# Kernel optimization log

Measured on AMD Instinct MI355X. Metric: run time of the kernel, lower is better.

Reference implementation:

```python
import jax, jax.numpy as jnp
import numpy as np

B, NQ, NK, QS, KS, H, VD = 16, 64, 512, 256, 256, 256, 256


def setup_inputs() -> dict:
    key = jax.random.key(0)
    k1, k2, k3, k4, k5, k6, k7 = jax.random.split(key, 7)
    return {
        "queries": jax.random.normal(k1, (B, NQ, QS), dtype=jnp.float32),
        "keys": jax.random.normal(k2, (B, NK, KS), dtype=jnp.float32),
        "values": jax.random.normal(k3, (B, NK, VD), dtype=jnp.float32),
        "valid_lens": jax.random.randint(k4, (B,), 1, NK + 1, dtype=jnp.int32),
        # learned params (nn.Linear with bias=False): W_q [QS,H], W_k [KS,H], w_v [H]
        "W_q": jax.random.normal(k5, (QS, H), dtype=jnp.float32) / np.sqrt(QS),
        "W_k": jax.random.normal(k6, (KS, H), dtype=jnp.float32) / np.sqrt(KS),
        "w_v": jax.random.normal(k7, (H,), dtype=jnp.float32) / np.sqrt(H),
    }


def reference(queries, keys, values, valid_lens, W_q, W_k, w_v):
    # project: q [B,nq,H], k [B,nk,H]
    q = jnp.einsum("bqd,dh->bqh", queries, W_q)
    k = jnp.einsum("bkd,dh->bkh", keys, W_k)
    # broadcast-add -> tanh -> score reduction via w_v: [B,nq,nk]
    features = jnp.tanh(q[:, :, None, :] + k[:, None, :, :])  # [B,nq,nk,H]
    scores = jnp.einsum("bqkh,h->bqk", features, w_v)
    # masked softmax over keys (positions >= valid_len masked out)
    mask = jnp.arange(scores.shape[-1])[None, None, :] < valid_lens[:, None, None]
    scores = jnp.where(mask, scores, -1e6)
    attn = jax.nn.softmax(scores, axis=-1)
    # weighted sum of values (dropout p=0 / eval mode => identity)
    return jnp.einsum("bqk,bkv->bqv", attn, values)
```

## Files before the change

kernel.cpp:

```cpp
#include <hip/hip_runtime.h>
#include <hip/hip_bf16.h>

#define BB 16
#define NQ 64
#define NK 512
#define HD 256

typedef __attribute__((ext_vector_type(8))) short short8;
typedef __attribute__((ext_vector_type(4))) float f32x4;

__device__ __forceinline__ ushort bf16_rne(float v) {
    unsigned u = __float_as_uint(v);
    return (ushort)((u + 0x7FFFu + ((u >> 16) & 1u)) >> 16);
}
__device__ __forceinline__ float bf16_to_f(ushort h) {
    return __uint_as_float(((unsigned)h) << 16);
}

__global__ __launch_bounds__(256) void wconv(
    const float* __restrict__ wq, const float* __restrict__ wk,
    ushort* __restrict__ wqh, ushort* __restrict__ wql,
    ushort* __restrict__ wkh, ushort* __restrict__ wkl)
{
    int widx = blockIdx.x * 256 + threadIdx.x;
    const float* W; ushort *wh, *wl;
    if (widx < 16384) { W = wq; wh = wqh; wl = wql; }
    else { W = wk; wh = wkh; wl = wkl; widx -= 16384; }
    int n  = widx >> 6;
    int k4 = (widx & 63) * 4;
    ushort hh[4], ll[4];
    #pragma unroll
    for (int c = 0; c < 4; ++c) {
        float v = W[(k4 + c) * 256 + n];
        hh[c] = bf16_rne(v);
        ll[c] = bf16_rne(v - bf16_to_f(hh[c]));
    }
    *(ushort4*)&wh[n * 256 + k4] = make_ushort4(hh[0], hh[1], hh[2], hh[3]);
    *(ushort4*)&wl[n * 256 + k4] = make_ushort4(ll[0], ll[1], ll[2], ll[3]);
}

__global__ __launch_bounds__(256, 2) void proj_fused(
    const float* __restrict__ queries, const float* __restrict__ keys,
    const ushort* __restrict__ wqh, const ushort* __restrict__ wql,
    const ushort* __restrict__ wkh, const ushort* __restrict__ wkl,
    float* __restrict__ qp, float* __restrict__ kp, float scale)
{
    __shared__ ushort AsH[64 * 64], AsL[64 * 64];
    __shared__ ushort BsH[64 * 64], BsL[64 * 64];

    const float* A; const ushort *Bh, *Bl; float* C; int rows0;
    const int bx = blockIdx.x;
    if (bx < 16) { A = queries; Bh = wqh; Bl = wql; C = qp; rows0 = bx * 64; }
    else         { A = keys;    Bh = wkh; Bl = wkl; C = kp; rows0 = (bx - 16) * 64; }
    const int cols0 = blockIdx.y * 64;

    const int t = threadIdx.x, lane = t & 63, wave = t >> 6;
    const int quad = lane >> 4, l15 = lane & 15;
    const int sr  = t >> 2;
    const int sc2 = (t & 3) * 2;

    f32x4 acc[4];
    #pragma unroll
    for (int j = 0; j < 4; ++j) acc[j] = (f32x4){0.f, 0.f, 0.f, 0.f};

    for (int k0 = 0; k0 < 256; k0 += 64) {
        const float* arow = &A[(size_t)(rows0 + sr) * 256 + k0 + sc2 * 8];
        float4 a0 = *(const float4*)&arow[0];
        float4 a1 = *(const float4*)&arow[4];
        float4 a2 = *(const float4*)&arow[8];
        float4 a3 = *(const float4*)&arow[12];
        const ushort* bhp = &Bh[(size_t)(cols0 + sr) * 256 + k0 + sc2 * 8];
        const ushort* blp = &Bl[(size_t)(cols0 + sr) * 256 + k0 + sc2 * 8];
        short8 b0h = *(const short8*)&bhp[0];
        short8 b1h = *(const short8*)&bhp[8];
        short8 b0l = *(const short8*)&blp[0];
        short8 b1l = *(const short8*)&blp[8];

        __syncthreads();

        float av[16] = {a0.x, a0.y, a0.z, a0.w, a1.x, a1.y, a1.z, a1.w,
                        a2.x, a2.y, a2.z, a2.w, a3.x, a3.y, a3.z, a3.w};
        short8 ah0, ah1, al0, al1;
        #pragma unroll
        for (int e = 0; e < 8; ++e) {
            ushort h0 = bf16_rne(av[e]);
            ushort h1 = bf16_rne(av[8 + e]);
            ah0[e] = (short)h0;
            ah1[e] = (short)h1;
            al0[e] = (short)bf16_rne(av[e] - bf16_to_f(h0));
            al1[e] = (short)bf16_rne(av[8 + e] - bf16_to_f(h1));
        }
        {
            int s0 = sr * 8 + ((sc2 + 0) ^ (sr & 7));
            int s1 = sr * 8 + ((sc2 + 1) ^ (sr & 7));
            *(short8*)&AsH[s0 * 8] = ah0;
            *(short8*)&AsH[s1 * 8] = ah1;
            *(short8*)&AsL[s0 * 8] = al0;
            *(short8*)&AsL[s1 * 8] = al1;
            *(short8*)&BsH[s0 * 8] = b0h;
            *(short8*)&BsH[s1 * 8] = b1h;
            *(short8*)&BsL[s0 * 8] = b0l;
            *(short8*)&BsL[s1 * 8] = b1l;
        }
        __syncthreads();

        #pragma unroll
        for (int ks = 0; ks < 2; ++ks) {
            const int c = ks * 4 + quad;
            short8 aH, aL, bH[4], bL[4];
            {
                int r = wave * 16 + l15;
                int slot = r * 8 + (c ^ (r & 7));
                aH = *(const short8*)&AsH[slot * 8];
                aL = *(const short8*)&AsL[slot * 8];
            }
            #pragma unroll
            for (int ns = 0; ns < 4; ++ns) {
                int n = ns * 16 + l15;
                int slot = n * 8 + (c ^ (n & 7));
                bH[ns] = *(const short8*)&BsH[slot * 8];
                bL[ns] = *(const short8*)&BsL[slot * 8];
            }
            #pragma unroll
            for (int ns = 0; ns < 4; ++ns)
                acc[ns] = __builtin_amdgcn_mfma_f32_16x16x32_bf16(aH, bH[ns], acc[ns], 0, 0, 0);
            #pragma unroll
            for (int ns = 0; ns < 4; ++ns)
                acc[ns] = __builtin_amdgcn_mfma_f32_16x16x32_bf16(aL, bH[ns], acc[ns], 0, 0, 0);
            #pragma unroll
            for (int ns = 0; ns < 4; ++ns)
                acc[ns] = __builtin_amdgcn_mfma_f32_16x16x32_bf16(aH, bL[ns], acc[ns], 0, 0, 0);
        }
    }

    const int rbase = rows0 + wave * 16 + quad * 4;
    #pragma unroll
    for (int ns = 0; ns < 4; ++ns) {
        int col = cols0 + ns * 16 + l15;
        #pragma unroll
        for (int r = 0; r < 4; ++r)
            C[(size_t)(rbase + r) * 256 + col] =
                __builtin_amdgcn_exp2f(acc[ns][r] * scale);
    }
}

__global__ __launch_bounds__(256, 3) void score_pv_seg4(
    const float* __restrict__ qp,
    const float* __restrict__ kp,
    const float* __restrict__ values,
    const int*   __restrict__ vlens,
    const float* __restrict__ w_v,
    float* __restrict__ pO,
    float* __restrict__ pL)
{
    __shared__ float eq[8][260];
    __shared__ float wv[HD];
    __shared__ float Ps[8][66];
    __shared__ float part[4][8][260];

    const int b   = blockIdx.x & 15;
    const int qt  = blockIdx.x >> 4;
    const int seg = blockIdx.y;
    const int vl  = vlens[b];
    if (seg * 64 >= vl) return;

    const int t = threadIdx.x, lane = t & 63, wave = t >> 6;
    const int key = wave * 16 + (lane >> 2);
    const int ch  = lane & 3;
    const int kg  = seg * 64 + key;

    const float* krow = kp + ((size_t)b * NK + kg) * HD + ch * 4;
    float4 ek[16];
    #pragma unroll
    for (int j = 0; j < 16; ++j) ek[j] = *(const float4*)&krow[j * 16];

    const float* qsrc = qp + ((size_t)b * NQ + qt * 8) * HD;
    #pragma unroll
    for (int i = 0; i < 2; ++i) {
        int idx = i * 256 + t;
        int row = idx >> 6, c4 = (idx & 63) * 4;
        *(float4*)&eq[row][c4] = *(const float4*)&qsrc[(size_t)row * HD + c4];
    }
    if (t < 64) *(float4*)&wv[t * 4] = *(const float4*)&w_v[t * 4];
    __syncthreads();

    float Wsum;
    {
        float ws = wv[lane] + wv[lane + 64] + wv[lane + 128] + wv[lane + 192];
        #pragma unroll
        for (int off = 32; off; off >>= 1) ws += __shfl_xor(ws, off);
        Wsum = ws;
    }

    float s[8] = {0.f, 0.f, 0.f, 0.f, 0.f, 0.f, 0.f, 0.f};
    #pragma unroll
    for (int j = 0; j < 16; ++j) {
        const int h = j * 16 + ch * 4;
        float4 e4 = ek[j];
        float4 w4 = *(const float4*)&wv[h];
        #pragma unroll
        for (int qi = 0; qi < 8; ++qi) {
            float4 q4 = *(const float4*)&eq[qi][h];
            float p0 = fmaf(q4.x, e4.x, 1.f);
            float p1 = fmaf(q4.y, e4.y, 1.f);
            float p2 = fmaf(q4.z, e4.z, 1.f);
            float p3 = fmaf(q4.w, e4.w, 1.f);
            float d01 = p0 * p1;
            float d23 = p2 * p3;
            float n01 = fmaf(w4.x, p1, w4.y * p0);
            float n23 = fmaf(w4.z, p3, w4.w * p2);
            float num = fmaf(d01, n23, d23 * n01);
            float r   = __builtin_amdgcn_rcpf(d01 * d23);
            s[qi] = fmaf(num, r, s[qi]);
        }
    }

    const float* vbase = values + ((size_t)b * NK + seg * 64 + wave * 16) * HD;
    float4 vv[16];
    #pragma unroll
    for (int i = 0; i < 16; ++i)
        vv[i] = *(const float4*)&vbase[(size_t)i * HD + lane * 4];

    const float L2E = 1.4426950408889634f;
    #pragma unroll
    for (int qi = 0; qi < 8; ++qi) {
        s[qi] += __shfl_xor(s[qi], 1);
        s[qi] += __shfl_xor(s[qi], 2);
    }
    if (ch == 0) {
        const bool masked = (kg >= vl);
        #pragma unroll
        for (int qi = 0; qi < 8; ++qi) {
            float sv = fmaf(-2.f, s[qi], Wsum);
            Ps[qi][key] = masked ? 0.f
                                 : __builtin_amdgcn_exp2f(sv * L2E);
        }
    }
    __syncthreads();

    f32x4 acc[8];
    #pragma unroll
    for (int qi = 0; qi < 8; ++qi) acc[qi] = (f32x4){0.f, 0.f, 0.f, 0.f};
    #pragma unroll
    for (int i = 0; i < 16; ++i) {
        float4 v = vv[i];
        #pragma unroll
        for (int qi = 0; qi < 8; ++qi) {
            float p = Ps[qi][wave * 16 + i];
            acc[qi][0] = fmaf(p, v.x, acc[qi][0]);
            acc[qi][1] = fmaf(p, v.y, acc[qi][1]);
            acc[qi][2] = fmaf(p, v.z, acc[qi][2]);
            acc[qi][3] = fmaf(p, v.w, acc[qi][3]);
        }
    }

    #pragma unroll
    for (int r = 0; r < 2; ++r) {
        const int row = wave * 2 + r;
        float l = Ps[row][lane];
        #pragma unroll
        for (int off = 32; off; off >>= 1) l += __shfl_xor(l, off);
        if (lane == 0)
            pL[(((size_t)(b * 8 + qt) * 8 + seg)) * 8 + row] = l;
    }

    #pragma unroll
    for (int qi = 0; qi < 8; ++qi)
        *(f32x4*)&part[wave][qi][lane * 4] = acc[qi];
    __syncthreads();

    const size_t ob = (((size_t)(b * 8 + qt) * 8 + seg)) * 8 * 256;
    #pragma unroll
    for (int i = 0; i < 2; ++i) {
        int idx = i * 256 + t;
        int qi = idx >> 6, c4 = (idx & 63) * 4;
        float4 p0 = *(const float4*)&part[0][qi][c4];
        float4 p1 = *(const float4*)&part[1][qi][c4];
        float4 p2 = *(const float4*)&part[2][qi][c4];
        float4 p3 = *(const float4*)&part[3][qi][c4];
        float4 o;
        o.x = (p0.x + p1.x) + (p2.x + p3.x);
        o.y = (p0.y + p1.y) + (p2.y + p3.y);
        o.z = (p0.z + p1.z) + (p2.z + p3.z);
        o.w = (p0.w + p1.w) + (p2.w + p3.w);
        *(float4*)&pO[ob + (size_t)qi * 256 + c4] = o;
    }
}

__global__ __launch_bounds__(256) void combine_seg3(
    const float* __restrict__ pO, const float* __restrict__ pL,
    const int* __restrict__ vlens, float* __restrict__ out)
{
    const int b  = blockIdx.x >> 6;
    const int q  = blockIdx.x & 63;
    const int t  = threadIdx.x;
    const int nc = (vlens[b] + 63) >> 6;
    const int qt = q >> 3, qi = q & 7;

    const size_t base = (size_t)(b * 8 + qt) * 8;

    float L = 0.f, acc = 0.f;
    #pragma unroll
    for (int i = 0; i < 8; ++i) {
        if (i < nc) {
            L   += pL[(base + i) * 8 + qi];
            acc += pO[((base + i) * 8 + qi) * 256 + t];
        }
    }
    out[((size_t)(b * 64 + q)) * 256 + t] = acc * __builtin_amdgcn_rcpf(L);
}

extern "C" void kernel_launch(void* const* d_in, const int* in_sizes, int n_in,
                              void* d_out, int out_size, void* d_ws, size_t ws_size,
                              hipStream_t stream) {
    const float* queries = (const float*)d_in[0];
    const float* keys    = (const float*)d_in[1];
    const float* values  = (const float*)d_in[2];
    const int*   vlens   = (const int*)d_in[3];
    const float* W_q     = (const float*)d_in[4];
    const float* W_k     = (const float*)d_in[5];
    const float* w_v     = (const float*)d_in[6];
    float* out = (float*)d_out;

    float*  kp  = (float*)d_ws;
    float*  qp  = kp + (size_t)BB * NK * HD;
    float*  pO  = qp + (size_t)BB * NQ * HD;
    float*  pL  = pO + (size_t)BB * 8 * 8 * 8 * 256;
    ushort* wqh = (ushort*)(pL + (size_t)BB * 8 * 8 * 8);
    ushort* wql = wqh + 65536;
    ushort* wkh = wql + 65536;
    ushort* wkl = wkh + 65536;

    const float SC = 2.885390081777927f;

    wconv<<<dim3(128), 256, 0, stream>>>(W_q, W_k, wqh, wql, wkh, wkl);
    proj_fused<<<dim3(144, 4), 256, 0, stream>>>(queries, keys,
                                                 wqh, wql, wkh, wkl,
                                                 qp, kp, SC);
    score_pv_seg4<<<dim3(128, 8), 256, 0, stream>>>(qp, kp, values, vlens, w_v,
                                                    pO, pL);
    combine_seg3<<<dim3(BB * NQ), 256, 0, stream>>>(pO, pL, vlens, out);
}
```

Baseline: 120.7 us.

## Split score and PV into separate kernels, write unnormalized probabilities to workspace

The fused score+PV kernel with per-segment partial outputs and a separate combine kernel is replaced by two kernels. A score-only kernel writes exp scores into a transposed probability buffer and runs at higher occupancy because it no longer needs the large LDS partial buffer. A PV kernel then streams values against the full key range per batch, reduces the softmax denominator itself and writes normalized output directly, so the partial-output round trip and the combine launch go away. The cost is that values are read once per query tile in the PV kernel, and its serial loop over keys may have limited parallelism with only 512 blocks.

```diff
diff --git a/kernel.cpp b/kernel.cpp
--- a/kernel.cpp
+++ b/kernel.cpp
@@ -144,19 +144,15 @@
     }
 }
 
-__global__ __launch_bounds__(256, 3) void score_pv_seg4(
+__global__ __launch_bounds__(256, 4) void score_a(
     const float* __restrict__ qp,
     const float* __restrict__ kp,
-    const float* __restrict__ values,
     const int*   __restrict__ vlens,
     const float* __restrict__ w_v,
-    float* __restrict__ pO,
-    float* __restrict__ pL)
+    float* __restrict__ Pt)
 {
     __shared__ float eq[8][260];
     __shared__ float wv[HD];
-    __shared__ float Ps[8][66];
-    __shared__ float part[4][8][260];
 
     const int b   = blockIdx.x & 15;
     const int qt  = blockIdx.x >> 4;
@@ -214,100 +210,81 @@
             s[qi] = fmaf(num, r, s[qi]);
         }
     }
-
-    const float* vbase = values + ((size_t)b * NK + seg * 64 + wave * 16) * HD;
-    float4 vv[16];
-    #pragma unroll
-    for (int i = 0; i < 16; ++i)
-        vv[i] = *(const float4*)&vbase[(size_t)i * HD + lane * 4];
-
-    const float L2E = 1.4426950408889634f;
     #pragma unroll
     for (int qi = 0; qi < 8; ++qi) {
         s[qi] += __shfl_xor(s[qi], 1);
         s[qi] += __shfl_xor(s[qi], 2);
     }
+
     if (ch == 0) {
         const bool masked = (kg >= vl);
+        const float L2E = 1.4426950408889634f;
+        float pt[8];
         #pragma unroll
         for (int qi = 0; qi < 8; ++qi) {
             float sv = fmaf(-2.f, s[qi], Wsum);
-            Ps[qi][key] = masked ? 0.f
-                                 : __builtin_amdgcn_exp2f(sv * L2E);
-        }
+            pt[qi] = masked ? 0.f : __builtin_amdgcn_exp2f(sv * L2E);
+        }
+        float* dst = &Pt[((size_t)b * NK + kg) * 64 + qt * 8];
+        *(float4*)&dst[0] = make_float4(pt[0], pt[1], pt[2], pt[3]);
+        *(float4*)&dst[4] = make_float4(pt[4], pt[5], pt[6], pt[7]);
+    }
+}
+
+__global__ __launch_bounds__(256) void pv_b(
+    const float* __restrict__ Pt,
+    const float* __restrict__ values,
+    const int*   __restrict__ vlens,
+    float* __restrict__ out)
+{
+    __shared__ f32x4 red[128];
+    __shared__ float Lred[8];
+    __shared__ float Lfin[8];
+
+    const int bx  = blockIdx.x;
+    const int b   = bx & 15;
+    const int qt  = (bx >> 4) & 7;
+    const int vdq = bx >> 7;
+    const int vl  = vlens[b];
+    const int nk  = ((vl + 63) >> 6) << 6;
+
+    const int t   = threadIdx.x;
+    const int vd4 = t & 15;
+    const int q   = (t >> 4) & 7;
+    const int kp2 = t >> 7;
+
+    const float* vptr = values + (size_t)b * NK * HD + vdq * 64 + vd4 * 4;
+    const float* pptr = Pt + (size_t)b * NK * 64 + qt * 8 + q;
+
+    f32x4 acc = (f32x4){0.f, 0.f, 0.f, 0.f};
+    float Lacc = 0.f;
+    #pragma unroll 8
+    for (int k = kp2; k < nk; k += 2) {
+        float  p = pptr[(size_t)k * 64];
+        float4 v = *(const float4*)&vptr[(size_t)k * HD];
+        acc[0] = fmaf(p, v.x, acc[0]);
+        acc[1] = fmaf(p, v.y, acc[1]);
+        acc[2] = fmaf(p, v.z, acc[2]);
+        acc[3] = fmaf(p, v.w, acc[3]);
+        Lacc += p;
+    }
+
+    if (kp2 == 1) {
+        red[t - 128] = acc;
+        if (vd4 == 0) Lred[q] = Lacc;
     }
     __syncthreads();
-
-    f32x4 acc[8];
-    #pragma unroll
-    for (int qi = 0; qi < 8; ++qi) acc[qi] = (f32x4){0.f, 0.f, 0.f, 0.f};
-    #pragma unroll
-    for (int i = 0; i < 16; ++i) {
-        float4 v = vv[i];
-        #pragma unroll
-        for (int qi = 0; qi < 8; ++qi) {
-            float p = Ps[qi][wave * 16 + i];
-            acc[qi][0] = fmaf(p, v.x, acc[qi][0]);
-            acc[qi][1] = fmaf(p, v.y, acc[qi][1]);
-            acc[qi][2] = fmaf(p, v.z, acc[qi][2]);
-            acc[qi][3] = fmaf(p, v.w, acc[qi][3]);
-        }
-    }
-
-    #pragma unroll
-    for (int r = 0; r < 2; ++r) {
-        const int row = wave * 2 + r;
-        float l = Ps[row][lane];
-        #pragma unroll
-        for (int off = 32; off; off >>= 1) l += __shfl_xor(l, off);
-        if (lane == 0)
-            pL[(((size_t)(b * 8 + qt) * 8 + seg)) * 8 + row] = l;
-    }
-
-    #pragma unroll
-    for (int qi = 0; qi < 8; ++qi)
-        *(f32x4*)&part[wave][qi][lane * 4] = acc[qi];
+    if (kp2 == 0) {
+        f32x4 o = red[t];
+        acc[0] += o[0]; acc[1] += o[1]; acc[2] += o[2]; acc[3] += o[3];
+        if (vd4 == 0) Lfin[q] = Lacc + Lred[q];
+    }
     __syncthreads();
-
-    const size_t ob = (((size_t)(b * 8 + qt) * 8 + seg)) * 8 * 256;
-    #pragma unroll
-    for (int i = 0; i < 2; ++i) {
-        int idx = i * 256 + t;
-        int qi = idx >> 6, c4 = (idx & 63) * 4;
-        float4 p0 = *(const float4*)&part[0][qi][c4];
-        float4 p1 = *(const float4*)&part[1][qi][c4];
-        float4 p2 = *(const float4*)&part[2][qi][c4];
-        float4 p3 = *(const float4*)&part[3][qi][c4];
-        float4 o;
-        o.x = (p0.x + p1.x) + (p2.x + p3.x);
-        o.y = (p0.y + p1.y) + (p2.y + p3.y);
-        o.z = (p0.z + p1.z) + (p2.z + p3.z);
-        o.w = (p0.w + p1.w) + (p2.w + p3.w);
-        *(float4*)&pO[ob + (size_t)qi * 256 + c4] = o;
-    }
-}
-
-__global__ __launch_bounds__(256) void combine_seg3(
-    const float* __restrict__ pO, const float* __restrict__ pL,
-    const int* __restrict__ vlens, float* __restrict__ out)
-{
-    const int b  = blockIdx.x >> 6;
-    const int q  = blockIdx.x & 63;
-    const int t  = threadIdx.x;
-    const int nc = (vlens[b] + 63) >> 6;
-    const int qt = q >> 3, qi = q & 7;
-
-    const size_t base = (size_t)(b * 8 + qt) * 8;
-
-    float L = 0.f, acc = 0.f;
-    #pragma unroll
-    for (int i = 0; i < 8; ++i) {
-        if (i < nc) {
-            L   += pL[(base + i) * 8 + qi];
-            acc += pO[((base + i) * 8 + qi) * 256 + t];
-        }
-    }
-    out[((size_t)(b * 64 + q)) * 256 + t] = acc * __builtin_amdgcn_rcpf(L);
+    if (kp2 == 0) {
+        float r = __builtin_amdgcn_rcpf(Lfin[q]);
+        float4 o = make_float4(acc[0] * r, acc[1] * r, acc[2] * r, acc[3] * r);
+        *(float4*)&out[((size_t)(b * 64 + qt * 8 + q)) * 256 + vdq * 64 + vd4 * 4] = o;
+    }
 }
 
 extern "C" void kernel_launch(void* const* d_in, const int* in_sizes, int n_in,
@@ -324,9 +301,8 @@
 
     float*  kp  = (float*)d_ws;
     float*  qp  = kp + (size_t)BB * NK * HD;
-    float*  pO  = qp + (size_t)BB * NQ * HD;
-    float*  pL  = pO + (size_t)BB * 8 * 8 * 8 * 256;
-    ushort* wqh = (ushort*)(pL + (size_t)BB * 8 * 8 * 8);
+    float*  Pt  = qp + (size_t)BB * NQ * HD;
+    ushort* wqh = (ushort*)(Pt + (size_t)BB * NK * 64);
     ushort* wql = wqh + 65536;
     ushort* wkh = wql + 65536;
     ushort* wkl = wkh + 65536;
@@ -337,7 +313,6 @@
     proj_fused<<<dim3(144, 4), 256, 0, stream>>>(queries, keys,
                                                  wqh, wql, wkh, wkl,
                                                  qp, kp, SC);
-    score_pv_seg4<<<dim3(128, 8), 256, 0, stream>>>(qp, kp, values, vlens, w_v,
-                                                    pO, pL);
-    combine_seg3<<<dim3(BB * NQ), 256, 0, stream>>>(pO, pL, vlens, out);
-}
+    score_a<<<dim3(128, 8), 256, 0, stream>>>(qp, kp, vlens, w_v, Pt);
+    pv_b<<<dim3(512), 256, 0, stream>>>(Pt, values, vlens, out);
+}
```

Measured after the change: 123.0 us. About the same (+1.9%).
